# Kernel tuning notes

Measured on AMD Instinct MI355X. Metric: run time of the kernel, lower is better.

## Reference

```python
import jax, jax.numpy as jnp
import numpy as np
import math

WINDOW = 2048
EMBED = 1024
BATCH = 8


def setup_inputs() -> dict:
    key = jax.random.key(0)
    ks = jax.random.split(key, 7)
    s = 1.0 / math.sqrt(EMBED)
    return {
        "embeddings": jax.random.normal(ks[0], (BATCH, WINDOW, EMBED), dtype=jnp.float32),
        "Wq": jax.random.uniform(ks[1], (EMBED, EMBED), jnp.float32, -s, s),
        "bq": jax.random.uniform(ks[2], (EMBED,), jnp.float32, -s, s),
        "Wk": jax.random.uniform(ks[3], (EMBED, EMBED), jnp.float32, -s, s),
        "bk": jax.random.uniform(ks[4], (EMBED,), jnp.float32, -s, s),
        "Wv": jax.random.uniform(ks[5], (EMBED, EMBED), jnp.float32, -s, s),
        "bv": jax.random.uniform(ks[6], (EMBED,), jnp.float32, -s, s),
    }


def reference(embeddings, Wq, bq, Wk, bk, Wv, bv):
    # Linear layers: x @ W.T + b (torch nn.Linear convention)
    Q = jnp.einsum('bse,fe->bsf', embeddings, Wq) + bq
    K = jnp.einsum('bse,fe->bsf', embeddings, Wk) + bk
    V = jnp.einsum('bse,fe->bsf', embeddings, Wv) + bv
    scale = 1.0 / math.sqrt(EMBED)
    # [B, S, S] score matrix: A[b, i, j] = Q_i . K_j / sqrt(d)
    A = jnp.einsum('bie,bje->bij', Q, K) * scale
    # causal additive mask: -inf where j > i (strictly upper triangular)
    mask = jnp.triu(jnp.full((WINDOW, WINDOW), -jnp.inf, dtype=A.dtype), k=1)
    A = A + mask
    # NOTE: faithful to original nn.Softmax(dim=1): normalize over QUERY axis
    P = jax.nn.softmax(A, axis=1)
    return jnp.einsum('bij,bje->bie', P, V)
```

## Files before the change

### kernel.cpp

```cpp
#include <hip/hip_runtime.h>
#include <stdint.h>

#define WINDOW 2048
#define EMBED  1024
#define BATCH  8
#define MTOT   (BATCH*WINDOW)

typedef unsigned short u16;
typedef __bf16 bf16x8 __attribute__((ext_vector_type(8)));
typedef float  f32x4  __attribute__((ext_vector_type(4)));

#define BK 64
#define KSCALE 0.04508422717564447f

#define BM2 256
#define BN2 256
#define HALF2 8192

#define BMR 128
#define BNR 256
#define AHALFR 4096
#define BHALFR 8192

#define WAITVM4 asm volatile("s_waitcnt vmcnt(4)" ::: "memory")
#define WAITVM3 asm volatile("s_waitcnt vmcnt(3)" ::: "memory")
#define WAITVM0 asm volatile("s_waitcnt vmcnt(0)" ::: "memory")
#define SBAR    __builtin_amdgcn_s_barrier()

__device__ __forceinline__ u16 f2bf(float f) {
  union { float f; unsigned u; } a; a.f = f;
  unsigned r = a.u + 0x7FFF + ((a.u >> 16) & 1);
  return (u16)(r >> 16);
}
__device__ __forceinline__ float bf2f(u16 u) {
  union { unsigned u; float f; } a; a.u = ((unsigned)u) << 16;
  return a.f;
}

__device__ __forceinline__ void gload16(const u16* g, u16* l) {
  __builtin_amdgcn_global_load_lds(
      (const __attribute__((address_space(1))) unsigned int*)g,
      (__attribute__((address_space(3))) unsigned int*)l, 16, 0, 0);
}


__device__ __forceinline__ void gemm256(
    const u16* __restrict__ A, int lda,
    const u16* __restrict__ B, int ldb,
    int nt, u16* lds, f32x4 acc[8][4])
{
  const int tid  = threadIdx.x;
  const int lane = tid & 63;
  const int wid  = tid >> 6;
  const int wm   = (wid >> 2) * 128;
  const int wn   = (wid & 3) * 64;
  const int lrow = lane & 15;
  const int hi   = lane >> 4;
  u16* dA = lds;
  u16* dB = lds + 4 * HALF2;

  int aoff[8], boff[4];
  #pragma unroll
  for (int mi = 0; mi < 8; ++mi) {
    int r = wm + mi * 16 + lrow;
    aoff[mi] = r * 32 + ((hi ^ ((r >> 1) & 3)) << 3);
  }
  #pragma unroll
  for (int ni = 0; ni < 4; ++ni) {
    int r = wn + ni * 16 + lrow;
    boff[ni] = r * 32 + ((hi ^ ((r >> 1) & 3)) << 3);
  }

  const int f0 = tid, f1 = 512 + tid;
  const int r0 = f0 >> 2, r1 = f1 >> 2;
  const int c0 = (((f0 & 3) ^ ((r0 >> 1) & 3)) << 3);
  const int c1 = (((f1 & 3) ^ ((r1 >> 1) & 3)) << 3);
  const u16* pA0 = A + (size_t)r0 * lda + c0;
  const u16* pA1 = A + (size_t)r1 * lda + c1;
  const u16* pB0 = B + (size_t)r0 * ldb + c0;
  const u16* pB1 = B + (size_t)r1 * ldb + c1;
  const int d0 = f0 * 8, d1 = f1 * 8;

  gload16(pA0,      dA + d0);         gload16(pA1,      dA + d1);
  gload16(pB0,      dB + d0);         gload16(pB1,      dB + d1);
  gload16(pA0 + 32, dA + HALF2 + d0); gload16(pA1 + 32, dA + HALF2 + d1);
  gload16(pB0 + 32, dB + HALF2 + d0); gload16(pB1 + 32, dB + HALF2 + d1);
  pA0 += BK; pA1 += BK; pB0 += BK; pB1 += BK;
  WAITVM4;
  SBAR;

  for (int t = 0; t < nt; ++t) {
    const int cb = (t & 1) * 2;
    const int nb = ((t + 1) & 1) * 2;
    u16* LA0 = dA + cb * HALF2;  u16* LA1 = LA0 + HALF2;
    u16* LB0 = dB + cb * HALF2;  u16* LB1 = LB0 + HALF2;
    const bool s = (t + 1) < nt;
    bf16x8 av[8], bv[4];

    #pragma unroll
    for (int mi = 0; mi < 8; ++mi) av[mi] = *(const bf16x8*)(LA0 + aoff[mi]);
    #pragma unroll
    for (int ni = 0; ni < 4; ++ni) bv[ni] = *(const bf16x8*)(LB0 + boff[ni]);
    if (s) {
      gload16(pA0, dA + nb * HALF2 + d0); gload16(pA1, dA + nb * HALF2 + d1);
      gload16(pB0, dB + nb * HALF2 + d0); gload16(pB1, dB + nb * HALF2 + d1);
    }
    __builtin_amdgcn_s_setprio(1);
    #pragma unroll
    for (int mi = 0; mi < 8; ++mi)
      #pragma unroll
      for (int ni = 0; ni < 4; ++ni)
        acc[mi][ni] = __builtin_amdgcn_mfma_f32_16x16x32_bf16(av[mi], bv[ni], acc[mi][ni], 0, 0, 0);
    __builtin_amdgcn_s_setprio(0);
    if (s) { WAITVM4; } else { WAITVM0; }
    SBAR;

    #pragma unroll
    for (int mi = 0; mi < 8; ++mi) av[mi] = *(const bf16x8*)(LA1 + aoff[mi]);
    #pragma unroll
    for (int ni = 0; ni < 4; ++ni) bv[ni] = *(const bf16x8*)(LB1 + boff[ni]);
    if (s) {
      gload16(pA0 + 32, dA + nb * HALF2 + HALF2 + d0); gload16(pA1 + 32, dA + nb * HALF2 + HALF2 + d1);
      gload16(pB0 + 32, dB + nb * HALF2 + HALF2 + d0); gload16(pB1 + 32, dB + nb * HALF2 + HALF2 + d1);
      pA0 += BK; pA1 += BK; pB0 += BK; pB1 += BK;
    }
    __builtin_amdgcn_s_setprio(1);
    #pragma unroll
    for (int mi = 0; mi < 8; ++mi)
      #pragma unroll
      for (int ni = 0; ni < 4; ++ni)
        acc[mi][ni] = __builtin_amdgcn_mfma_f32_16x16x32_bf16(av[mi], bv[ni], acc[mi][ni], 0, 0, 0);
    __builtin_amdgcn_s_setprio(0);
    if (s) { WAITVM4; }
    SBAR;
  }
}

__device__ __forceinline__ void gemm_rect(
    const u16* __restrict__ A, int lda,
    const u16* __restrict__ B, int ldb,
    int nt, u16* lds, f32x4 acc[4][4])
{
  const int tid  = threadIdx.x;
  const int lane = tid & 63;
  const int wid  = tid >> 6;
  const int wm   = (wid >> 2) * 64;
  const int wn   = (wid & 3) * 64;
  const int lrow = lane & 15;
  const int hi   = lane >> 4;
  u16* dA = lds;
  u16* dB = lds + 4 * AHALFR;

  int aoff[4], boff[4];
  #pragma unroll
  for (int mi = 0; mi < 4; ++mi) {
    int r = wm + mi * 16 + lrow;
    aoff[mi] = r * 32 + ((hi ^ ((r >> 1) & 3)) << 3);
  }
  #pragma unroll
  for (int ni = 0; ni < 4; ++ni) {
    int r = wn + ni * 16 + lrow;
    boff[ni] = r * 32 + ((hi ^ ((r >> 1) & 3)) << 3);
  }

  const int fa = tid;
  const int fb0 = tid, fb1 = 512 + tid;
  const int ra = fa >> 2, rb0 = fb0 >> 2, rb1 = fb1 >> 2;
  const int ca  = (((fa  & 3) ^ ((ra  >> 1) & 3)) << 3);
  const int cb0 = (((fb0 & 3) ^ ((rb0 >> 1) & 3)) << 3);
  const int cb1 = (((fb1 & 3) ^ ((rb1 >> 1) & 3)) << 3);
  const u16* pA  = A + (size_t)ra  * lda + ca;
  const u16* pB0 = B + (size_t)rb0 * ldb + cb0;
  const u16* pB1 = B + (size_t)rb1 * ldb + cb1;
  const int da = fa * 8, db0 = fb0 * 8, db1 = fb1 * 8;

  gload16(pA,       dA + da);
  gload16(pB0,      dB + db0);          gload16(pB1,      dB + db1);
  gload16(pA + 32,  dA + AHALFR + da);
  gload16(pB0 + 32, dB + BHALFR + db0); gload16(pB1 + 32, dB + BHALFR + db1);
  pA += BK; pB0 += BK; pB1 += BK;
  WAITVM3;
  SBAR;

  for (int t = 0; t < nt; ++t) {
    const int cb = (t & 1) * 2;
    const int nb = ((t + 1) & 1) * 2;
    u16* LA0 = dA + cb * AHALFR;  u16* LA1 = LA0 + AHALFR;
    u16* LB0 = dB + cb * BHALFR;  u16* LB1 = LB0 + BHALFR;
    const bool s = (t + 1) < nt;
    bf16x8 av[4], bv[4];

    #pragma unroll
    for (int mi = 0; mi < 4; ++mi) av[mi] = *(const bf16x8*)(LA0 + aoff[mi]);
    #pragma unroll
    for (int ni = 0; ni < 4; ++ni) bv[ni] = *(const bf16x8*)(LB0 + boff[ni]);
    if (s) {
      gload16(pA,  dA + nb * AHALFR + da);
      gload16(pB0, dB + nb * BHALFR + db0); gload16(pB1, dB + nb * BHALFR + db1);
    }
    __builtin_amdgcn_s_setprio(1);
    #pragma unroll
    for (int mi = 0; mi < 4; ++mi)
      #pragma unroll
      for (int ni = 0; ni < 4; ++ni)
        acc[mi][ni] = __builtin_amdgcn_mfma_f32_16x16x32_bf16(av[mi], bv[ni], acc[mi][ni], 0, 0, 0);
    __builtin_amdgcn_s_setprio(0);
    if (s) { WAITVM3; } else { WAITVM0; }
    SBAR;

    #pragma unroll
    for (int mi = 0; mi < 4; ++mi) av[mi] = *(const bf16x8*)(LA1 + aoff[mi]);
    #pragma unroll
    for (int ni = 0; ni < 4; ++ni) bv[ni] = *(const bf16x8*)(LB1 + boff[ni]);
    if (s) {
      gload16(pA + 32,  dA + nb * AHALFR + AHALFR + da);
      gload16(pB0 + 32, dB + nb * BHALFR + BHALFR + db0);
      gload16(pB1 + 32, dB + nb * BHALFR + BHALFR + db1);
      pA += BK; pB0 += BK; pB1 += BK;
    }
    __builtin_amdgcn_s_setprio(1);
    #pragma unroll
    for (int mi = 0; mi < 4; ++mi)
      #pragma unroll
      for (int ni = 0; ni < 4; ++ni)
        acc[mi][ni] = __builtin_amdgcn_mfma_f32_16x16x32_bf16(av[mi], bv[ni], acc[mi][ni], 0, 0, 0);
    __builtin_amdgcn_s_setprio(0);
    if (s) { WAITVM3; }
    SBAR;
  }
}

__global__ __launch_bounds__(256) void k_cvt(const float* __restrict__ in,
                                             u16* __restrict__ out, int n) {
  int i = (blockIdx.x * 256 + threadIdx.x) * 4;
  if (i >= n) return;
  float4 v = *(const float4*)(in + i);
  ushort4 o;
  o.x = f2bf(v.x); o.y = f2bf(v.y); o.z = f2bf(v.z); o.w = f2bf(v.w);
  *(ushort4*)(out + i) = o;
}

__global__ __launch_bounds__(512, 2) void k_qkv(
    const u16* __restrict__ Xb, const u16* __restrict__ Wb,
    const float* __restrict__ bq, const float* __restrict__ bk, const float* __restrict__ bv,
    u16* __restrict__ Q, u16* __restrict__ Ks, u16* __restrict__ V)
{
  __shared__ u16 lds[8 * HALF2];
  const int m0 = blockIdx.x * BM2;
  const int n0 = blockIdx.y * BN2;
  const int z  = blockIdx.z;
  const u16*   W    = Wb + (size_t)z * EMBED * EMBED;
  const float* bias = (z == 0) ? bq : (z == 1) ? bk : bv;
  u16* out          = (z == 0) ? Q  : (z == 1) ? Ks : V;
  const float scale = (z == 1) ? KSCALE : 1.0f;

  f32x4 acc[8][4];
  const f32x4 zz = {0.f,0.f,0.f,0.f};
  #pragma unroll
  for (int i = 0; i < 8; ++i) for (int j = 0; j < 4; ++j) acc[i][j] = zz;
  gemm256(Xb + (size_t)m0 * EMBED, EMBED, W + (size_t)n0 * EMBED, EMBED,
          EMBED / BK, lds, acc);

  const int lane = threadIdx.x & 63, wid = threadIdx.x >> 6;
  const int wm = (wid >> 2) * 128, wn = (wid & 3) * 64;
  const int lrow = lane & 15, hi = lane >> 4;
  #pragma unroll
  for (int mi = 0; mi < 8; ++mi)
    #pragma unroll
    for (int ni = 0; ni < 4; ++ni)
      #pragma unroll
      for (int rr = 0; rr < 4; ++rr) {
        int gm = m0 + wm + mi * 16 + hi * 4 + rr;
        int gn = n0 + wn + ni * 16 + lrow;
        out[(size_t)gm * EMBED + gn] = f2bf((acc[mi][ni][rr] + bias[gn]) * scale);
      }
}

__global__ __launch_bounds__(512, 2) void k_spd(
    const u16* __restrict__ Q, const u16* __restrict__ Ks,
    u16* __restrict__ P, float* __restrict__ D)
{
  const int ii = blockIdx.x;
  const int jj = blockIdx.y;
  const int i0 = ii * BMR;
  const int j0 = jj * BNR;
  if (j0 > i0 + (BMR - 1)) return;
  const int b  = blockIdx.z;
  __shared__ u16 lds[4 * AHALFR + 4 * BHALFR];
  const u16* A = Q  + (size_t)b * WINDOW * EMBED + (size_t)i0 * EMBED;
  const u16* B = Ks + (size_t)b * WINDOW * EMBED + (size_t)j0 * EMBED;
  f32x4 acc[4][4];
  const f32x4 zz = {0.f,0.f,0.f,0.f};
  #pragma unroll
  for (int i = 0; i < 4; ++i) for (int j = 0; j < 4; ++j) acc[i][j] = zz;
  gemm_rect(A, EMBED, B, EMBED, EMBED / BK, lds, acc);

  u16* Pb   = P + (size_t)b * WINDOW * WINDOW;
  float* Db = D + (size_t)b * WINDOW;
  const int lane = threadIdx.x & 63, wid = threadIdx.x >> 6;
  const int wm = (wid >> 2) * 64, wn = (wid & 3) * 64;
  const int lrow = lane & 15, hi = lane >> 4;
  #pragma unroll
  for (int ni = 0; ni < 4; ++ni) {
    int gj = j0 + wn + ni * 16 + lrow;
    float csum = 0.f;
    #pragma unroll
    for (int mi = 0; mi < 4; ++mi)
      #pragma unroll
      for (int rr = 0; rr < 4; ++rr) {
        int gi = i0 + wm + mi * 16 + hi * 4 + rr;
        float p = (gi >= gj) ? exp2f(acc[mi][ni][rr]) : 0.0f;
        Pb[(size_t)gi * WINDOW + gj] = f2bf(p);
        csum += p;
      }
    csum += __shfl_xor(csum, 16, 64);
    csum += __shfl_xor(csum, 32, 64);
    if (hi == 0) atomicAdd(&Db[gj], csum);
  }
}

__global__ __launch_bounds__(256) void k_vdt(
    const u16* __restrict__ V, const float* __restrict__ D, u16* __restrict__ Vdt)
{
  __shared__ u16 tile[64][68];
  const int j0 = blockIdx.x * 64, e0 = blockIdx.y * 64, b = blockIdx.z;
  const u16* Vb = V   + (size_t)b * WINDOW * EMBED;
  u16* Tb       = Vdt + (size_t)b * EMBED * WINDOW;
  const float* Db = D + (size_t)b * WINDOW;
  const int t = threadIdx.x;
  const int rr = t >> 4;
  const int cc = (t & 15) * 4;
  #pragma unroll
  for (int p = 0; p < 4; ++p) {
    int r = p * 16 + rr;
    *(uint2*)&tile[r][cc] = *(const uint2*)(Vb + (size_t)(j0 + r) * EMBED + e0 + cc);
  }
  __syncthreads();
  #pragma unroll
  for (int p = 0; p < 4; ++p) {
    int er = p * 16 + rr;
    ushort4 o;
    o.x = f2bf(bf2f(tile[cc + 0][er]) / Db[j0 + cc + 0]);
    o.y = f2bf(bf2f(tile[cc + 1][er]) / Db[j0 + cc + 1]);
    o.z = f2bf(bf2f(tile[cc + 2][er]) / Db[j0 + cc + 2]);
    o.w = f2bf(bf2f(tile[cc + 3][er]) / Db[j0 + cc + 3]);
    *(ushort4*)(Tb + (size_t)(e0 + er) * WINDOW + j0 + cc) = o;
  }
}

__global__ __launch_bounds__(512, 2) void k_out(
    const u16* __restrict__ P, const u16* __restrict__ Vdt, float* __restrict__ O)
{
  __shared__ u16 lds[4 * AHALFR + 4 * BHALFR];
  const int ii = (int)gridDim.x - 1 - (int)blockIdx.x;
  const int i0 = ii * BMR;
  const int e0 = blockIdx.y * BNR;
  const int b  = blockIdx.z;
  const u16* A = P   + (size_t)b * WINDOW * WINDOW + (size_t)i0 * WINDOW;
  const u16* B = Vdt + (size_t)b * EMBED * WINDOW  + (size_t)e0 * WINDOW;
  f32x4 acc[4][4];
  const f32x4 zz = {0.f,0.f,0.f,0.f};
  #pragma unroll
  for (int i = 0; i < 4; ++i) for (int j = 0; j < 4; ++j) acc[i][j] = zz;
  gemm_rect(A, WINDOW, B, WINDOW, (i0 + BMR) / BK, lds, acc);

  float* Ob = O + (size_t)b * WINDOW * EMBED;
  const int lane = threadIdx.x & 63, wid = threadIdx.x >> 6;
  const int wm = (wid >> 2) * 64, wn = (wid & 3) * 64;
  const int lrow = lane & 15, hi = lane >> 4;
  #pragma unroll
  for (int mi = 0; mi < 4; ++mi)
    #pragma unroll
    for (int ni = 0; ni < 4; ++ni)
      #pragma unroll
      for (int rr = 0; rr < 4; ++rr) {
        int gi = i0 + wm + mi * 16 + hi * 4 + rr;
        int ge = e0 + wn + ni * 16 + lrow;
        Ob[(size_t)gi * EMBED + ge] = acc[mi][ni][rr];
      }
}

extern "C" void kernel_launch(void* const* d_in, const int* in_sizes, int n_in,
                              void* d_out, int out_size, void* d_ws, size_t ws_size,
                              hipStream_t stream) {
  const float* X  = (const float*)d_in[0];
  const float* Wq = (const float*)d_in[1];
  const float* bq = (const float*)d_in[2];
  const float* Wk = (const float*)d_in[3];
  const float* bk = (const float*)d_in[4];
  const float* Wv = (const float*)d_in[5];
  const float* bv = (const float*)d_in[6];
  float* O = (float*)d_out;

  char* ws = (char*)d_ws;
  size_t off = 0;
  auto alloc = [&](size_t bytes) -> void* {
    void* p = ws + off; off += (bytes + 255) & ~(size_t)255; return p;
  };
  u16*  Xb  = (u16*)alloc((size_t)MTOT * EMBED * 2);
  u16*  Wb  = (u16*)alloc((size_t)3 * EMBED * EMBED * 2);
  u16*  Qb  = (u16*)alloc((size_t)MTOT * EMBED * 2);
  u16*  Kb  = (u16*)alloc((size_t)MTOT * EMBED * 2);
  u16*  Vb  = (u16*)alloc((size_t)MTOT * EMBED * 2);
  u16*  Vdt = (u16*)alloc((size_t)BATCH * EMBED * WINDOW * 2);
  u16*  P   = (u16*)alloc((size_t)BATCH * WINDOW * WINDOW * 2);
  float* D  = (float*)alloc((size_t)MTOT * 4);
  (void)ws_size; (void)in_sizes; (void)n_in; (void)out_size;

  k_cvt<<<dim3((MTOT * EMBED / 4 + 255) / 256), 256, 0, stream>>>(X, Xb, MTOT * EMBED);
  k_cvt<<<dim3((EMBED * EMBED / 4 + 255) / 256), 256, 0, stream>>>(Wq, Wb, EMBED * EMBED);
  k_cvt<<<dim3((EMBED * EMBED / 4 + 255) / 256), 256, 0, stream>>>(Wk, Wb + (size_t)EMBED * EMBED, EMBED * EMBED);
  k_cvt<<<dim3((EMBED * EMBED / 4 + 255) / 256), 256, 0, stream>>>(Wv, Wb + (size_t)2 * EMBED * EMBED, EMBED * EMBED);

  k_qkv<<<dim3(MTOT / BM2, EMBED / BN2, 3), 512, 0, stream>>>(Xb, Wb, bq, bk, bv, Qb, Kb, Vb);

  (void)hipMemsetAsync(D, 0, (size_t)MTOT * 4, stream);
  k_spd<<<dim3(WINDOW / BMR, WINDOW / BNR, BATCH), 512, 0, stream>>>(Qb, Kb, P, D);

  k_vdt<<<dim3(WINDOW / 64, EMBED / 64, BATCH), 256, 0, stream>>>(Vb, D, Vdt);

  k_out<<<dim3(WINDOW / BMR, EMBED / BNR, BATCH), 512, 0, stream>>>(P, Vdt, O);
}
```

Baseline: 308.9 us.

## Use 256x256 tiles with XCD-aware triangular scheduling for score and output GEMMs

The score kernel now launches a flat grid that maps only lower-triangular 256x256 tiles, swizzled so each XCD works on one batch. It stages P through padded LDS to get coalesced 16-byte stores, and handles the diagonal-adjacent last tiles with 128-row rect blocks. The output GEMM switches to 256x256 tiles with a flat XCD-swizzled grid ordered longest-first, and the three weight conversions are merged into one launch. The aim is better operand reuse, no early-exit blocks, and better L2 locality, at the cost of bigger tiles, which may reduce parallelism and leave the grid imbalanced.

```diff
diff --git a/kernel.cpp b/kernel.cpp
--- a/kernel.cpp
+++ b/kernel.cpp
@@ -16,9 +16,8 @@
 #define BM2 256
 #define BN2 256
 #define HALF2 8192
-
-#define BMR 128
-#define BNR 256
+#define PLD  260
+
 #define AHALFR 4096
 #define BHALFR 8192
 
@@ -240,6 +239,19 @@
   *(ushort4*)(out + i) = o;
 }
 
+__global__ __launch_bounds__(256) void k_cvtw(const float* __restrict__ w0,
+                                              const float* __restrict__ w1,
+                                              const float* __restrict__ w2,
+                                              u16* __restrict__ out) {
+  const float* in = (blockIdx.y == 0) ? w0 : (blockIdx.y == 1) ? w1 : w2;
+  u16* o = out + (size_t)blockIdx.y * EMBED * EMBED;
+  int i = (blockIdx.x * 256 + threadIdx.x) * 4;
+  float4 v = *(const float4*)(in + i);
+  ushort4 r;
+  r.x = f2bf(v.x); r.y = f2bf(v.y); r.z = f2bf(v.z); r.w = f2bf(v.w);
+  *(ushort4*)(o + i) = r;
+}
+
 __global__ __launch_bounds__(512, 2) void k_qkv(
     const u16* __restrict__ Xb, const u16* __restrict__ Wb,
     const float* __restrict__ bq, const float* __restrict__ bk, const float* __restrict__ bv,
@@ -280,42 +292,102 @@
     const u16* __restrict__ Q, const u16* __restrict__ Ks,
     u16* __restrict__ P, float* __restrict__ D)
 {
-  const int ii = blockIdx.x;
-  const int jj = blockIdx.y;
-  const int i0 = ii * BMR;
-  const int j0 = jj * BNR;
-  if (j0 > i0 + (BMR - 1)) return;
-  const int b  = blockIdx.z;
-  __shared__ u16 lds[4 * AHALFR + 4 * BHALFR];
-  const u16* A = Q  + (size_t)b * WINDOW * EMBED + (size_t)i0 * EMBED;
-  const u16* B = Ks + (size_t)b * WINDOW * EMBED + (size_t)j0 * EMBED;
-  f32x4 acc[4][4];
-  const f32x4 zz = {0.f,0.f,0.f,0.f};
-  #pragma unroll
-  for (int i = 0; i < 4; ++i) for (int j = 0; j < 4; ++j) acc[i][j] = zz;
-  gemm_rect(A, EMBED, B, EMBED, EMBED / BK, lds, acc);
-
-  u16* Pb   = P + (size_t)b * WINDOW * WINDOW;
-  float* Db = D + (size_t)b * WINDOW;
-  const int lane = threadIdx.x & 63, wid = threadIdx.x >> 6;
-  const int wm = (wid >> 2) * 64, wn = (wid & 3) * 64;
-  const int lrow = lane & 15, hi = lane >> 4;
-  #pragma unroll
-  for (int ni = 0; ni < 4; ++ni) {
-    int gj = j0 + wn + ni * 16 + lrow;
-    float csum = 0.f;
-    #pragma unroll
-    for (int mi = 0; mi < 4; ++mi)
-      #pragma unroll
-      for (int rr = 0; rr < 4; ++rr) {
-        int gi = i0 + wm + mi * 16 + hi * 4 + rr;
-        float p = (gi >= gj) ? exp2f(acc[mi][ni][rr]) : 0.0f;
-        Pb[(size_t)gi * WINDOW + gj] = f2bf(p);
-        csum += p;
-      }
-    csum += __shfl_xor(csum, 16, 64);
-    csum += __shfl_xor(csum, 32, 64);
-    if (hi == 0) atomicAdd(&Db[gj], csum);
+  __shared__ u16 lds[BM2 * PLD];
+  const int sblk = blockIdx.x;
+
+  if (sblk < 256) {
+    const int xcd = sblk & 7;
+    const int q   = sblk >> 3;
+    int it = 0;
+    while (q >= ((it + 1) * (it + 2)) / 2) ++it;
+    const int jt = q - (it * (it + 1)) / 2;
+    const int b  = (xcd - it) & 7;
+    const int i0 = it * BM2;
+    const int j0 = jt * BN2;
+
+    const u16* A = Q  + (size_t)b * WINDOW * EMBED + (size_t)i0 * EMBED;
+    const u16* B = Ks + (size_t)b * WINDOW * EMBED + (size_t)j0 * EMBED;
+    f32x4 acc[8][4];
+    const f32x4 zz = {0.f,0.f,0.f,0.f};
+    #pragma unroll
+    for (int i = 0; i < 8; ++i) for (int j = 0; j < 4; ++j) acc[i][j] = zz;
+    gemm256(A, EMBED, B, EMBED, EMBED / BK, lds, acc);
+
+    u16* Pb   = P + (size_t)b * WINDOW * WINDOW;
+    float* Db = D + (size_t)b * WINDOW;
+    const int tid  = threadIdx.x;
+    const int lane = tid & 63, wid = tid >> 6;
+    const int wm = (wid >> 2) * 128, wn = (wid & 3) * 64;
+    const int lrow = lane & 15, hi = lane >> 4;
+
+    #pragma unroll
+    for (int ni = 0; ni < 4; ++ni) {
+      int lj = wn + ni * 16 + lrow;
+      float csum = 0.f;
+      #pragma unroll
+      for (int mi = 0; mi < 8; ++mi)
+        #pragma unroll
+        for (int rr = 0; rr < 4; ++rr) {
+          int li = wm + mi * 16 + hi * 4 + rr;
+          float p = ((i0 + li) >= (j0 + lj)) ? exp2f(acc[mi][ni][rr]) : 0.0f;
+          lds[li * PLD + lj] = f2bf(p);
+          csum += p;
+        }
+      csum += __shfl_xor(csum, 16, 64);
+      csum += __shfl_xor(csum, 32, 64);
+      if (hi == 0) atomicAdd(&Db[j0 + lj], csum);
+    }
+    __syncthreads();
+
+    #pragma unroll
+    for (int it2 = 0; it2 < 16; ++it2) {
+      int f   = it2 * 512 + tid;
+      int row = f >> 5;
+      int c   = f & 31;
+      bf16x8 v = *(const bf16x8*)(lds + row * PLD + c * 8);
+      *(bf16x8*)(Pb + (size_t)(i0 + row) * WINDOW + j0 + c * 8) = v;
+    }
+  } else {
+    const int ih   = sblk - 256;
+    const int xcd  = ih & 7;
+    const int h    = ih >> 3;
+    const int jt   = 4 + (h >> 1);
+    const int half = h & 1;
+    const int it   = 7;
+    const int b    = (xcd - it) & 7;
+    const int i0   = it * BM2 + half * 128;
+    const int j0   = jt * BN2;
+
+    const u16* A = Q  + (size_t)b * WINDOW * EMBED + (size_t)i0 * EMBED;
+    const u16* B = Ks + (size_t)b * WINDOW * EMBED + (size_t)j0 * EMBED;
+    f32x4 acc[4][4];
+    const f32x4 zz = {0.f,0.f,0.f,0.f};
+    #pragma unroll
+    for (int i = 0; i < 4; ++i) for (int j = 0; j < 4; ++j) acc[i][j] = zz;
+    gemm_rect(A, EMBED, B, EMBED, EMBED / BK, lds, acc);
+
+    u16* Pb   = P + (size_t)b * WINDOW * WINDOW;
+    float* Db = D + (size_t)b * WINDOW;
+    const int lane = threadIdx.x & 63, wid = threadIdx.x >> 6;
+    const int wm = (wid >> 2) * 64, wn = (wid & 3) * 64;
+    const int lrow = lane & 15, hi = lane >> 4;
+    #pragma unroll
+    for (int ni = 0; ni < 4; ++ni) {
+      int gj = j0 + wn + ni * 16 + lrow;
+      float csum = 0.f;
+      #pragma unroll
+      for (int mi = 0; mi < 4; ++mi)
+        #pragma unroll
+        for (int rr = 0; rr < 4; ++rr) {
+          int gi = i0 + wm + mi * 16 + hi * 4 + rr;
+          float p = (gi >= gj) ? exp2f(acc[mi][ni][rr]) : 0.0f;
+          Pb[(size_t)gi * WINDOW + gj] = f2bf(p);
+          csum += p;
+        }
+      csum += __shfl_xor(csum, 16, 64);
+      csum += __shfl_xor(csum, 32, 64);
+      if (hi == 0) atomicAdd(&Db[gj], csum);
+    }
   }
 }
 
@@ -351,25 +423,30 @@
 __global__ __launch_bounds__(512, 2) void k_out(
     const u16* __restrict__ P, const u16* __restrict__ Vdt, float* __restrict__ O)
 {
-  __shared__ u16 lds[4 * AHALFR + 4 * BHALFR];
-  const int ii = (int)gridDim.x - 1 - (int)blockIdx.x;
-  const int i0 = ii * BMR;
-  const int e0 = blockIdx.y * BNR;
-  const int b  = blockIdx.z;
+  __shared__ u16 lds[8 * HALF2];
+  const int s   = blockIdx.x;
+  const int xcd = s & 7;
+  const int q   = s >> 3;
+  const int et  = q & 3;
+  const int it  = 7 - (q >> 2);
+  const int b   = (xcd - it) & 7;
+  const int i0  = it * BM2;
+  const int e0  = et * BN2;
+
   const u16* A = P   + (size_t)b * WINDOW * WINDOW + (size_t)i0 * WINDOW;
   const u16* B = Vdt + (size_t)b * EMBED * WINDOW  + (size_t)e0 * WINDOW;
-  f32x4 acc[4][4];
+  f32x4 acc[8][4];
   const f32x4 zz = {0.f,0.f,0.f,0.f};
   #pragma unroll
-  for (int i = 0; i < 4; ++i) for (int j = 0; j < 4; ++j) acc[i][j] = zz;
-  gemm_rect(A, WINDOW, B, WINDOW, (i0 + BMR) / BK, lds, acc);
+  for (int i = 0; i < 8; ++i) for (int j = 0; j < 4; ++j) acc[i][j] = zz;
+  gemm256(A, WINDOW, B, WINDOW, (i0 + BM2) / BK, lds, acc);
 
   float* Ob = O + (size_t)b * WINDOW * EMBED;
   const int lane = threadIdx.x & 63, wid = threadIdx.x >> 6;
-  const int wm = (wid >> 2) * 64, wn = (wid & 3) * 64;
+  const int wm = (wid >> 2) * 128, wn = (wid & 3) * 64;
   const int lrow = lane & 15, hi = lane >> 4;
   #pragma unroll
-  for (int mi = 0; mi < 4; ++mi)
+  for (int mi = 0; mi < 8; ++mi)
     #pragma unroll
     for (int ni = 0; ni < 4; ++ni)
       #pragma unroll
@@ -408,16 +485,14 @@
   (void)ws_size; (void)in_sizes; (void)n_in; (void)out_size;
 
   k_cvt<<<dim3((MTOT * EMBED / 4 + 255) / 256), 256, 0, stream>>>(X, Xb, MTOT * EMBED);
-  k_cvt<<<dim3((EMBED * EMBED / 4 + 255) / 256), 256, 0, stream>>>(Wq, Wb, EMBED * EMBED);
-  k_cvt<<<dim3((EMBED * EMBED / 4 + 255) / 256), 256, 0, stream>>>(Wk, Wb + (size_t)EMBED * EMBED, EMBED * EMBED);
-  k_cvt<<<dim3((EMBED * EMBED / 4 + 255) / 256), 256, 0, stream>>>(Wv, Wb + (size_t)2 * EMBED * EMBED, EMBED * EMBED);
+  k_cvtw<<<dim3(EMBED * EMBED / 4 / 256, 3), 256, 0, stream>>>(Wq, Wk, Wv, Wb);
 
   k_qkv<<<dim3(MTOT / BM2, EMBED / BN2, 3), 512, 0, stream>>>(Xb, Wb, bq, bk, bv, Qb, Kb, Vb);
 
   (void)hipMemsetAsync(D, 0, (size_t)MTOT * 4, stream);
-  k_spd<<<dim3(WINDOW / BMR, WINDOW / BNR, BATCH), 512, 0, stream>>>(Qb, Kb, P, D);
+  k_spd<<<dim3(320), 512, 0, stream>>>(Qb, Kb, P, D);
 
   k_vdt<<<dim3(WINDOW / 64, EMBED / 64, BATCH), 256, 0, stream>>>(Vb, D, Vdt);
 
-  k_out<<<dim3(WINDOW / BMR, EMBED / BNR, BATCH), 512, 0, stream>>>(P, Vdt, O);
-}
+  k_out<<<dim3(256), 512, 0, stream>>>(P, Vdt, O);
+}
```

Measured after the change: 273.6 us. 1.13x faster.
